# Kernel optimization log

Hardware: AMD Instinct MI355X
Metric: run time of the kernel (lower is better)

## Reference

```python
import jax, jax.numpy as jnp
import numpy as np

IN_DIM, HIDDEN, OUT_DIM = 784, 2048, 10
BATCH = 16384
KEEP = 0.1  # 1 - sparsity


def setup_inputs() -> dict:
    key = jax.random.key(0)
    ks = jax.random.split(key, 16)
    s1 = 1.0 / np.sqrt(IN_DIM)
    sh = 1.0 / np.sqrt(HIDDEN)
    inp = {
        "x": jax.random.normal(ks[0], (BATCH, IN_DIM), dtype=jnp.float32),
        # weights stored as (out, in) like nn.Linear
        "W1": jax.random.uniform(ks[1], (HIDDEN, IN_DIM), jnp.float32, -s1, s1),
        "b1": jax.random.uniform(ks[2], (HIDDEN,), jnp.float32, -s1, s1),
        "W2": jax.random.uniform(ks[3], (HIDDEN, HIDDEN), jnp.float32, -sh, sh),
        "b2": jax.random.uniform(ks[4], (HIDDEN,), jnp.float32, -sh, sh),
        "W3": jax.random.uniform(ks[5], (HIDDEN, HIDDEN), jnp.float32, -sh, sh),
        "b3": jax.random.uniform(ks[6], (HIDDEN,), jnp.float32, -sh, sh),
        "W4": jax.random.uniform(ks[7], (HIDDEN, HIDDEN), jnp.float32, -sh, sh),
        "b4": jax.random.uniform(ks[8], (HIDDEN,), jnp.float32, -sh, sh),
        "W5": jax.random.uniform(ks[9], (OUT_DIM, HIDDEN), jnp.float32, -sh, sh),
        "b5": jax.random.uniform(ks[10], (OUT_DIM,), jnp.float32, -sh, sh),
        "m1": jax.random.bernoulli(ks[11], KEEP, (HIDDEN, IN_DIM)),
        "m2": jax.random.bernoulli(ks[12], KEEP, (HIDDEN, HIDDEN)),
        "m3": jax.random.bernoulli(ks[13], KEEP, (HIDDEN, HIDDEN)),
        "m4": jax.random.bernoulli(ks[14], KEEP, (HIDDEN, HIDDEN)),
    }
    return inp


def _sparse_linear(x, W, b, m):
    # masked linear: y = x @ (W*m)^T + b
    Wm = W * m.astype(W.dtype)
    return x @ Wm.T + b


def reference(x, W1, b1, W2, b2, W3, b3, W4, b4, W5, b5, m1, m2, m3, m4):
    h = x.reshape(x.shape[0], -1)
    h = jax.nn.relu(_sparse_linear(h, W1, b1, m1))
    h = jax.nn.relu(_sparse_linear(h, W2, b2, m2))
    h = jax.nn.relu(_sparse_linear(h, W3, b3, m3))
    h = jax.nn.relu(_sparse_linear(h, W4, b4, m4))
    return h @ W5.T + b5
```

## Files before the change

kernel.cpp:

```cpp
#include <hip/hip_runtime.h>
#include <hip/hip_bf16.h>
#include <hip/hip_fp16.h>

#define BATCH 16384
#define HID   2048
#define IND   784
#define INDP  896
#define OUTD  10

typedef _Float16 f16;
typedef __attribute__((ext_vector_type(8))) _Float16 f16x8;
typedef __attribute__((ext_vector_type(4))) float f32x4;

__global__ void mask_detect(const unsigned char* __restrict__ p, int nbytes,
                            int* __restrict__ flags) {
    int acc = 0;
    for (int i = blockIdx.x * blockDim.x + threadIdx.x; i < nbytes;
         i += gridDim.x * blockDim.x) {
        unsigned char b = p[i];
        if (b > 1) acc |= 2;
        else if (b != 0 && (i & 3) != 0) acc |= 1;
    }
    if (acc) atomicOr(flags, acc);
}

__global__ void prep_cast(const float* __restrict__ W,
                          const void* __restrict__ Mk,
                          const int* __restrict__ flags,
                          f16* __restrict__ out,
                          int rin, int kin, int kout, int total) {
    int idx = blockIdx.x * blockDim.x + threadIdx.x;
    if (idx >= total) return;
    int r = idx / kout, c = idx - r * kout;
    float v = 0.f;
    if (r < rin && c < kin) {
        v = W[(size_t)r * kin + c];
        if (Mk) {
            size_t mi = (size_t)r * kin + c;
            bool byteMode = (*flags == 1);
            bool keep = byteMode ? (((const unsigned char*)Mk)[mi] != 0)
                                 : (((const unsigned int*)Mk)[mi] != 0u);
            if (!keep) v = 0.f;
        }
    }
    out[idx] = (f16)v;
}

__device__ __forceinline__ void gload_lds16(const f16* g, f16* l) {
    __builtin_amdgcn_global_load_lds(
        (const __attribute__((address_space(1))) unsigned int*)g,
        (__attribute__((address_space(3))) unsigned int*)l,
        16, 0, 0);
}

#define BAR()    __builtin_amdgcn_s_barrier()
#define SCHED()  __builtin_amdgcn_sched_barrier(0)
#define WAITV4() asm volatile("s_waitcnt vmcnt(4)" ::: "memory")
#define WAITV8() asm volatile("s_waitcnt vmcnt(8)" ::: "memory")
#define WAITL0() asm volatile("s_waitcnt lgkmcnt(0)" ::: "memory")

template<bool RELU>
__global__ __launch_bounds__(512, 2) void gemm8p(
    const f16* __restrict__ A, const f16* __restrict__ B,
    const float* __restrict__ bias, f16* __restrict__ C,
    int N, int K) {
    __shared__ f16 As[2 * 2 * 256 * 32];
    __shared__ f16 Bs[2 * 2 * 256 * 32];

    int nbn = N >> 8;
    int nwg = gridDim.x;
    int cpx = nwg >> 3;
    int bid = blockIdx.x;
    int swz = (bid & 7) * cpx + (bid >> 3);
    int bm = swz / nbn, bn = swz % nbn;

    int tid = threadIdx.x;
    int w = tid >> 6, lane = tid & 63;
    int wr = w >> 2, wc = w & 3;
    int l15 = lane & 15, l4 = lane >> 4;

    const f16* Ag = A + (size_t)bm * 256 * K;
    const f16* Bg = B + (size_t)bn * 256 * K;

    int r0 = tid >> 2, s0 = tid & 3;
    int c0 = (s0 ^ ((r0 >> 1) & 3)) * 8;
    int ldsw0 = (w * 64) * 8;
    int ldsw1 = (512 + w * 64) * 8;

    auto stageA = [&](int buf, int ks, int tk) {
        const f16* s = Ag + (size_t)r0 * K + tk * 64 + ks * 32 + c0;
        gload_lds16(s, As + (buf * 2 + ks) * 8192 + ldsw0);
        const f16* s2 = Ag + (size_t)(128 + r0) * K + tk * 64 + ks * 32 + c0;
        gload_lds16(s2, As + (buf * 2 + ks) * 8192 + ldsw1);
    };
    auto stageB = [&](int buf, int ks, int tk) {
        const f16* s = Bg + (size_t)r0 * K + tk * 64 + ks * 32 + c0;
        gload_lds16(s, Bs + (buf * 2 + ks) * 8192 + ldsw0);
        const f16* s2 = Bg + (size_t)(128 + r0) * K + tk * 64 + ks * 32 + c0;
        gload_lds16(s2, Bs + (buf * 2 + ks) * 8192 + ldsw1);
    };

    int rsw = (l4 ^ ((l15 >> 1) & 3)) * 8;
    auto ldA = [&](f16x8 (&af)[4], int buf, int ks, int mh) {
        int base = (buf * 2 + ks) * 8192;
        #pragma unroll
        for (int m = 0; m < 4; ++m) {
            int row = wr * 128 + (mh * 4 + m) * 16 + l15;
            af[m] = *(const f16x8*)(As + base + row * 32 + rsw);
        }
    };
    auto ldB = [&](f16x8 (&bf)[4], int buf, int ks) {
        int base = (buf * 2 + ks) * 8192;
        #pragma unroll
        for (int n = 0; n < 4; ++n) {
            int row = wc * 64 + n * 16 + l15;
            bf[n] = *(const f16x8*)(Bs + base + row * 32 + rsw);
        }
    };

    f32x4 acc[8][4] = {};
    auto mma = [&](f16x8 (&af)[4], f16x8 (&bf)[4], int mh) {
        __builtin_amdgcn_s_setprio(1);
        #pragma unroll
        for (int m = 0; m < 4; ++m)
            #pragma unroll
            for (int n = 0; n < 4; ++n)
                acc[mh * 4 + m][n] = __builtin_amdgcn_mfma_f32_16x16x32_f16(
                    af[m], bf[n], acc[mh * 4 + m][n], 0, 0, 0);
        __builtin_amdgcn_s_setprio(0);
    };

    int NT = K >> 6, NI = NT >> 1;

    f16x8 A0[4], A1[4], B0[4], B1[4];

    stageA(0, 0, 0); stageB(0, 0, 0); stageA(0, 1, 0); stageB(0, 1, 0);
    stageA(1, 0, 1); stageB(1, 0, 1);
    WAITV8(); SCHED(); BAR();
    ldA(A0, 0, 0, 0); ldB(B0, 0, 0);
    WAITL0(); SCHED();

    for (int it = 0; it < NI; ++it) {
        int t1 = 2 * it + 1, t2 = 2 * it + 2, t3 = 2 * it + 3;
        if (t2 >= NT) t2 = 0;
        if (t3 >= NT) t3 = 0;

        ldA(A1, 0, 0, 1); stageA(1, 1, t1); SCHED();
        mma(A0, B0, 0);
        WAITL0(); WAITV4(); SCHED(); BAR();
        ldA(A0, 0, 1, 0); ldB(B1, 0, 1); stageB(1, 1, t1); SCHED();
        mma(A1, B0, 1);
        WAITL0(); SCHED(); BAR();
        ldA(A1, 0, 1, 1); stageA(0, 0, t2); SCHED();
        mma(A0, B1, 0);
        WAITL0(); WAITV4(); SCHED(); BAR();
        ldA(A0, 1, 0, 0); ldB(B0, 1, 0); stageB(0, 0, t2); SCHED();
        mma(A1, B1, 1);
        WAITL0(); SCHED(); BAR();
        ldA(A1, 1, 0, 1); stageA(0, 1, t2); SCHED();
        mma(A0, B0, 0);
        WAITL0(); WAITV4(); SCHED(); BAR();
        ldA(A0, 1, 1, 0); ldB(B1, 1, 1); stageB(0, 1, t2); SCHED();
        mma(A1, B0, 1);
        WAITL0(); SCHED(); BAR();
        ldA(A1, 1, 1, 1); stageA(1, 0, t3); SCHED();
        mma(A0, B1, 0);
        WAITL0(); WAITV4(); SCHED(); BAR();
        ldA(A0, 0, 0, 0); ldB(B0, 0, 0); stageB(1, 0, t3); SCHED();
        mma(A1, B1, 1);
        WAITL0(); SCHED(); BAR();
    }

    #pragma unroll
    for (int nf = 0; nf < 4; ++nf) {
        int j = bn * 256 + wc * 64 + nf * 16 + l15;
        float bv = bias[j];
        #pragma unroll
        for (int mf = 0; mf < 8; ++mf) {
            int i0 = bm * 256 + wr * 128 + mf * 16 + l4 * 4;
            #pragma unroll
            for (int r = 0; r < 4; ++r) {
                float v = acc[mf][nf][r] + bv;
                if (RELU) v = fmaxf(v, 0.f);
                C[(size_t)(i0 + r) * N + j] = (f16)v;
            }
        }
    }
}

__global__ __launch_bounds__(256, 3) void gemm_head(
    const f16* __restrict__ A, const f16* __restrict__ B,
    const float* __restrict__ bias, float* __restrict__ C,
    int K, int Nout) {
    __shared__ f16 As[128 * 64];
    __shared__ f16 Bs[128 * 64];
    int bm = blockIdx.x;
    int t = threadIdx.x;
    int w = t >> 6, lane = t & 63;
    int wm = w >> 1, wn = w & 1;
    int l15 = lane & 15, l4 = lane >> 4;
    const f16* Ag = A + (size_t)bm * 128 * K;
    const f16* Bg = B;
    int rr = w * 8 + (lane >> 3);
    int cc = (lane & 7) * 8;
    f32x4 acc[4][4] = {};
    for (int k0 = 0; k0 < K; k0 += 64) {
        #pragma unroll
        for (int i = 0; i < 4; ++i)
            gload_lds16(Ag + (size_t)(i * 32 + rr) * K + k0 + cc, As + i * 2048 + w * 512);
        #pragma unroll
        for (int i = 0; i < 4; ++i)
            gload_lds16(Bg + (size_t)(i * 32 + rr) * K + k0 + cc, Bs + i * 2048 + w * 512);
        __syncthreads();
        #pragma unroll
        for (int ks = 0; ks < 2; ++ks) {
            f16x8 af[4], bfr[4];
            #pragma unroll
            for (int m = 0; m < 4; ++m)
                af[m] = *(const f16x8*)(As + (wm * 64 + m * 16 + l15) * 64 + ks * 32 + l4 * 8);
            #pragma unroll
            for (int n = 0; n < 4; ++n)
                bfr[n] = *(const f16x8*)(Bs + (wn * 64 + n * 16 + l15) * 64 + ks * 32 + l4 * 8);
            #pragma unroll
            for (int m = 0; m < 4; ++m)
                #pragma unroll
                for (int n = 0; n < 4; ++n)
                    acc[m][n] = __builtin_amdgcn_mfma_f32_16x16x32_f16(af[m], bfr[n], acc[m][n], 0, 0, 0);
        }
        __syncthreads();
    }
    #pragma unroll
    for (int n = 0; n < 4; ++n) {
        int j = wn * 64 + n * 16 + l15;
        bool jok = j < Nout;
        float bv = jok ? bias[j] : 0.f;
        #pragma unroll
        for (int m = 0; m < 4; ++m) {
            int i0 = bm * 128 + wm * 64 + m * 16 + l4 * 4;
            #pragma unroll
            for (int r = 0; r < 4; ++r) {
                if (jok) C[(size_t)(i0 + r) * Nout + j] = acc[m][n][r] + bv;
            }
        }
    }
}

extern "C" void kernel_launch(void* const* d_in, const int* in_sizes, int n_in,
                              void* d_out, int out_size, void* d_ws, size_t ws_size,
                              hipStream_t stream) {
    const float* x  = (const float*)d_in[0];
    const float* W1 = (const float*)d_in[1];
    const float* b1 = (const float*)d_in[2];
    const float* W2 = (const float*)d_in[3];
    const float* b2 = (const float*)d_in[4];
    const float* W3 = (const float*)d_in[5];
    const float* b3 = (const float*)d_in[6];
    const float* W4 = (const float*)d_in[7];
    const float* b4 = (const float*)d_in[8];
    const float* W5 = (const float*)d_in[9];
    const float* b5 = (const float*)d_in[10];
    const void* m1 = d_in[11];
    const void* m2 = d_in[12];
    const void* m3 = d_in[13];
    const void* m4 = d_in[14];

    char* ws = (char*)d_ws;
    size_t off = 0;
    auto alloc = [&](size_t b) { char* p = ws + off; off += (b + 255) & ~(size_t)255; return p; };
    f16* xb  = (f16*)alloc((size_t)BATCH * INDP * 2);
    f16* w1b = (f16*)alloc((size_t)HID * INDP * 2);
    f16* w2b = (f16*)alloc((size_t)HID * HID * 2);
    f16* w3b = (f16*)alloc((size_t)HID * HID * 2);
    f16* w4b = (f16*)alloc((size_t)HID * HID * 2);
    f16* w5b = (f16*)alloc((size_t)128 * HID * 2);
    f16* h1  = (f16*)alloc((size_t)BATCH * HID * 2);
    f16* h2  = (f16*)alloc((size_t)BATCH * HID * 2);
    int* flags = (int*)alloc(256);

    hipMemsetAsync(flags, 0, sizeof(int), stream);
    mask_detect<<<64, 256, 0, stream>>>((const unsigned char*)m1, 262144, flags);

    auto prep = [&](const float* src, const void* mk, f16* dst,
                    int rin, int kin, int kout, int rout) {
        int total = rout * kout;
        prep_cast<<<(total + 255) / 256, 256, 0, stream>>>(src, mk, flags, dst,
                                                           rin, kin, kout, total);
    };
    prep(x,  nullptr, xb,  BATCH, IND, INDP, BATCH);
    prep(W1, m1,      w1b, HID,   IND, INDP, HID);
    prep(W2, m2,      w2b, HID,   HID, HID,  HID);
    prep(W3, m3,      w3b, HID,   HID, HID,  HID);
    prep(W4, m4,      w4b, HID,   HID, HID,  HID);
    prep(W5, nullptr, w5b, OUTD,  HID, HID,  128);

    int g8 = (BATCH / 256) * (HID / 256);
    gemm8p<true><<<g8, 512, 0, stream>>>(xb, w1b, b1, h1, HID, INDP);
    gemm8p<true><<<g8, 512, 0, stream>>>(h1, w2b, b2, h2, HID, HID);
    gemm8p<true><<<g8, 512, 0, stream>>>(h2, w3b, b3, h1, HID, HID);
    gemm8p<true><<<g8, 512, 0, stream>>>(h1, w4b, b4, h2, HID, HID);
    gemm_head<<<BATCH / 128, 256, 0, stream>>>(h2, w5b, b5, (float*)d_out, HID, OUTD);
}
```

Baseline: 562.4 us.

## Use 4-wave 256x256 GEMM workgroups with 128x128 per-wave tiles

Rewrites the main GEMM kernel from 8 waves (each computing a 128x64 sub-tile) to 4 waves each computing a 128x128 sub-tile of the same 256x256 block tile. Each thread now issues four global-to-LDS loads per stage instead of two, and the vmcnt waits are adjusted to match. The goal is more MFMA work per LDS fragment read and fewer waves contending for barriers. In exchange, accumulator register use doubles (256 fp32 per lane), occupancy drops to one workgroup of four waves per CU, and there is less latency hiding.

```diff
diff --git a/kernel.cpp b/kernel.cpp
--- a/kernel.cpp
+++ b/kernel.cpp
@@ -55,12 +55,11 @@
 
 #define BAR()    __builtin_amdgcn_s_barrier()
 #define SCHED()  __builtin_amdgcn_sched_barrier(0)
-#define WAITV4() asm volatile("s_waitcnt vmcnt(4)" ::: "memory")
 #define WAITV8() asm volatile("s_waitcnt vmcnt(8)" ::: "memory")
 #define WAITL0() asm volatile("s_waitcnt lgkmcnt(0)" ::: "memory")
 
 template<bool RELU>
-__global__ __launch_bounds__(512, 2) void gemm8p(
+__global__ __launch_bounds__(256, 1) void gemm4w(
     const f16* __restrict__ A, const f16* __restrict__ B,
     const float* __restrict__ bias, f16* __restrict__ C,
     int N, int K) {
@@ -76,7 +75,7 @@
 
     int tid = threadIdx.x;
     int w = tid >> 6, lane = tid & 63;
-    int wr = w >> 2, wc = w & 3;
+    int wr = w >> 1, wc = w & 1;
     int l15 = lane & 15, l4 = lane >> 4;
 
     const f16* Ag = A + (size_t)bm * 256 * K;
@@ -84,20 +83,18 @@
 
     int r0 = tid >> 2, s0 = tid & 3;
     int c0 = (s0 ^ ((r0 >> 1) & 3)) * 8;
-    int ldsw0 = (w * 64) * 8;
-    int ldsw1 = (512 + w * 64) * 8;
 
     auto stageA = [&](int buf, int ks, int tk) {
-        const f16* s = Ag + (size_t)r0 * K + tk * 64 + ks * 32 + c0;
-        gload_lds16(s, As + (buf * 2 + ks) * 8192 + ldsw0);
-        const f16* s2 = Ag + (size_t)(128 + r0) * K + tk * 64 + ks * 32 + c0;
-        gload_lds16(s2, As + (buf * 2 + ks) * 8192 + ldsw1);
+        #pragma unroll
+        for (int j = 0; j < 4; ++j)
+            gload_lds16(Ag + (size_t)(j * 64 + r0) * K + tk * 64 + ks * 32 + c0,
+                        As + (buf * 2 + ks) * 8192 + j * 2048 + w * 512);
     };
     auto stageB = [&](int buf, int ks, int tk) {
-        const f16* s = Bg + (size_t)r0 * K + tk * 64 + ks * 32 + c0;
-        gload_lds16(s, Bs + (buf * 2 + ks) * 8192 + ldsw0);
-        const f16* s2 = Bg + (size_t)(128 + r0) * K + tk * 64 + ks * 32 + c0;
-        gload_lds16(s2, Bs + (buf * 2 + ks) * 8192 + ldsw1);
+        #pragma unroll
+        for (int j = 0; j < 4; ++j)
+            gload_lds16(Bg + (size_t)(j * 64 + r0) * K + tk * 64 + ks * 32 + c0,
+                        Bs + (buf * 2 + ks) * 8192 + j * 2048 + w * 512);
     };
 
     int rsw = (l4 ^ ((l15 >> 1) & 3)) * 8;
@@ -109,22 +106,22 @@
             af[m] = *(const f16x8*)(As + base + row * 32 + rsw);
         }
     };
-    auto ldB = [&](f16x8 (&bf)[4], int buf, int ks) {
+    auto ldB = [&](f16x8 (&bf)[8], int buf, int ks) {
         int base = (buf * 2 + ks) * 8192;
         #pragma unroll
-        for (int n = 0; n < 4; ++n) {
-            int row = wc * 64 + n * 16 + l15;
+        for (int n = 0; n < 8; ++n) {
+            int row = wc * 128 + n * 16 + l15;
             bf[n] = *(const f16x8*)(Bs + base + row * 32 + rsw);
         }
     };
 
-    f32x4 acc[8][4] = {};
-    auto mma = [&](f16x8 (&af)[4], f16x8 (&bf)[4], int mh) {
+    f32x4 acc[8][8] = {};
+    auto mma = [&](f16x8 (&af)[4], f16x8 (&bf)[8], int mh) {
         __builtin_amdgcn_s_setprio(1);
         #pragma unroll
         for (int m = 0; m < 4; ++m)
             #pragma unroll
-            for (int n = 0; n < 4; ++n)
+            for (int n = 0; n < 8; ++n)
                 acc[mh * 4 + m][n] = __builtin_amdgcn_mfma_f32_16x16x32_f16(
                     af[m], bf[n], acc[mh * 4 + m][n], 0, 0, 0);
         __builtin_amdgcn_s_setprio(0);
@@ -132,7 +129,7 @@
 
     int NT = K >> 6, NI = NT >> 1;
 
-    f16x8 A0[4], A1[4], B0[4], B1[4];
+    f16x8 A0[4], A1[4], B0[8], B1[8];
 
     stageA(0, 0, 0); stageB(0, 0, 0); stageA(0, 1, 0); stageB(0, 1, 0);
     stageA(1, 0, 1); stageB(1, 0, 1);
@@ -147,33 +144,33 @@
 
         ldA(A1, 0, 0, 1); stageA(1, 1, t1); SCHED();
         mma(A0, B0, 0);
-        WAITL0(); WAITV4(); SCHED(); BAR();
+        WAITL0(); WAITV8(); SCHED(); BAR();
         ldA(A0, 0, 1, 0); ldB(B1, 0, 1); stageB(1, 1, t1); SCHED();
         mma(A1, B0, 1);
         WAITL0(); SCHED(); BAR();
         ldA(A1, 0, 1, 1); stageA(0, 0, t2); SCHED();
         mma(A0, B1, 0);
-        WAITL0(); WAITV4(); SCHED(); BAR();
+        WAITL0(); WAITV8(); SCHED(); BAR();
         ldA(A0, 1, 0, 0); ldB(B0, 1, 0); stageB(0, 0, t2); SCHED();
         mma(A1, B1, 1);
         WAITL0(); SCHED(); BAR();
         ldA(A1, 1, 0, 1); stageA(0, 1, t2); SCHED();
         mma(A0, B0, 0);
-        WAITL0(); WAITV4(); SCHED(); BAR();
+        WAITL0(); WAITV8(); SCHED(); BAR();
         ldA(A0, 1, 1, 0); ldB(B1, 1, 1); stageB(0, 1, t2); SCHED();
         mma(A1, B0, 1);
         WAITL0(); SCHED(); BAR();
         ldA(A1, 1, 1, 1); stageA(1, 0, t3); SCHED();
         mma(A0, B1, 0);
-        WAITL0(); WAITV4(); SCHED(); BAR();
+        WAITL0(); WAITV8(); SCHED(); BAR();
         ldA(A0, 0, 0, 0); ldB(B0, 0, 0); stageB(1, 0, t3); SCHED();
         mma(A1, B1, 1);
         WAITL0(); SCHED(); BAR();
     }
 
     #pragma unroll
-    for (int nf = 0; nf < 4; ++nf) {
-        int j = bn * 256 + wc * 64 + nf * 16 + l15;
+    for (int nf = 0; nf < 8; ++nf) {
+        int j = bn * 256 + wc * 128 + nf * 16 + l15;
         float bv = bias[j];
         #pragma unroll
         for (int mf = 0; mf < 8; ++mf) {
@@ -293,10 +290,10 @@
     prep(W4, m4,      w4b, HID,   HID, HID,  HID);
     prep(W5, nullptr, w5b, OUTD,  HID, HID,  128);
 
-    int g8 = (BATCH / 256) * (HID / 256);
-    gemm8p<true><<<g8, 512, 0, stream>>>(xb, w1b, b1, h1, HID, INDP);
-    gemm8p<true><<<g8, 512, 0, stream>>>(h1, w2b, b2, h2, HID, HID);
-    gemm8p<true><<<g8, 512, 0, stream>>>(h2, w3b, b3, h1, HID, HID);
-    gemm8p<true><<<g8, 512, 0, stream>>>(h1, w4b, b4, h2, HID, HID);
+    int g4 = (BATCH / 256) * (HID / 256);
+    gemm4w<true><<<g4, 256, 0, stream>>>(xb, w1b, b1, h1, HID, INDP);
+    gemm4w<true><<<g4, 256, 0, stream>>>(h1, w2b, b2, h2, HID, HID);
+    gemm4w<true><<<g4, 256, 0, stream>>>(h2, w3b, b3, h1, HID, HID);
+    gemm4w<true><<<g4, 256, 0, stream>>>(h1, w4b, b4, h2, HID, HID);
     gemm_head<<<BATCH / 128, 256, 0, stream>>>(h2, w5b, b5, (float*)d_out, HID, OUTD);
 }
```

Measured after the change: 604.2 us. 1.07x slower.

## Reorder GEMM main loop to issue MFMAs before next LDS fragment reads

Applied to the files above, without the earlier changes.

Restructures the software-pipelined main loop of the fp16 MFMA GEMM so each phase runs its MFMAs first and then issues the LDS fragment reads and global-to-LDS stages for the next phase. It also preloads both A halves in the prologue and drops the explicit lgkmcnt(0) waits, leaving LDS-read waits to the compiler. The aim is more overlap of LDS reads and global loads with MFMA work and fewer full stalls per phase. Without the explicit LDS-read waits before barriers, a wave's pending fragment reads could race with other waves' async writes into the same buffer.

```diff
diff --git a/kernel.cpp b/kernel.cpp
--- a/kernel.cpp
+++ b/kernel.cpp
@@ -57,7 +57,6 @@
 #define SCHED()  __builtin_amdgcn_sched_barrier(0)
 #define WAITV4() asm volatile("s_waitcnt vmcnt(4)" ::: "memory")
 #define WAITV8() asm volatile("s_waitcnt vmcnt(8)" ::: "memory")
-#define WAITL0() asm volatile("s_waitcnt lgkmcnt(0)" ::: "memory")
 
 template<bool RELU>
 __global__ __launch_bounds__(512, 2) void gemm8p(
@@ -88,16 +87,16 @@
     int ldsw1 = (512 + w * 64) * 8;
 
     auto stageA = [&](int buf, int ks, int tk) {
-        const f16* s = Ag + (size_t)r0 * K + tk * 64 + ks * 32 + c0;
-        gload_lds16(s, As + (buf * 2 + ks) * 8192 + ldsw0);
-        const f16* s2 = Ag + (size_t)(128 + r0) * K + tk * 64 + ks * 32 + c0;
-        gload_lds16(s2, As + (buf * 2 + ks) * 8192 + ldsw1);
+        gload_lds16(Ag + (size_t)r0 * K + tk * 64 + ks * 32 + c0,
+                    As + (buf * 2 + ks) * 8192 + ldsw0);
+        gload_lds16(Ag + (size_t)(128 + r0) * K + tk * 64 + ks * 32 + c0,
+                    As + (buf * 2 + ks) * 8192 + ldsw1);
     };
     auto stageB = [&](int buf, int ks, int tk) {
-        const f16* s = Bg + (size_t)r0 * K + tk * 64 + ks * 32 + c0;
-        gload_lds16(s, Bs + (buf * 2 + ks) * 8192 + ldsw0);
-        const f16* s2 = Bg + (size_t)(128 + r0) * K + tk * 64 + ks * 32 + c0;
-        gload_lds16(s2, Bs + (buf * 2 + ks) * 8192 + ldsw1);
+        gload_lds16(Bg + (size_t)r0 * K + tk * 64 + ks * 32 + c0,
+                    Bs + (buf * 2 + ks) * 8192 + ldsw0);
+        gload_lds16(Bg + (size_t)(128 + r0) * K + tk * 64 + ks * 32 + c0,
+                    Bs + (buf * 2 + ks) * 8192 + ldsw1);
     };
 
     int rsw = (l4 ^ ((l15 >> 1) & 3)) * 8;
@@ -132,43 +131,43 @@
 
     int NT = K >> 6, NI = NT >> 1;
 
-    f16x8 A0[4], A1[4], B0[4], B1[4];
+    f16x8 Aa[4], Ab[4], Ba[4], Bb[4];
 
     stageA(0, 0, 0); stageB(0, 0, 0); stageA(0, 1, 0); stageB(0, 1, 0);
     stageA(1, 0, 1); stageB(1, 0, 1);
     WAITV8(); SCHED(); BAR();
-    ldA(A0, 0, 0, 0); ldB(B0, 0, 0);
-    WAITL0(); SCHED();
+    ldA(Aa, 0, 0, 0); ldB(Bb, 0, 0); ldA(Ab, 0, 0, 1);
+    WAITV4(); SCHED(); BAR();
 
     for (int it = 0; it < NI; ++it) {
         int t1 = 2 * it + 1, t2 = 2 * it + 2, t3 = 2 * it + 3;
         if (t2 >= NT) t2 = 0;
         if (t3 >= NT) t3 = 0;
 
-        ldA(A1, 0, 0, 1); stageA(1, 1, t1); SCHED();
-        mma(A0, B0, 0);
-        WAITL0(); WAITV4(); SCHED(); BAR();
-        ldA(A0, 0, 1, 0); ldB(B1, 0, 1); stageB(1, 1, t1); SCHED();
-        mma(A1, B0, 1);
-        WAITL0(); SCHED(); BAR();
-        ldA(A1, 0, 1, 1); stageA(0, 0, t2); SCHED();
-        mma(A0, B1, 0);
-        WAITL0(); WAITV4(); SCHED(); BAR();
-        ldA(A0, 1, 0, 0); ldB(B0, 1, 0); stageB(0, 0, t2); SCHED();
-        mma(A1, B1, 1);
-        WAITL0(); SCHED(); BAR();
-        ldA(A1, 1, 0, 1); stageA(0, 1, t2); SCHED();
-        mma(A0, B0, 0);
-        WAITL0(); WAITV4(); SCHED(); BAR();
-        ldA(A0, 1, 1, 0); ldB(B1, 1, 1); stageB(0, 1, t2); SCHED();
-        mma(A1, B0, 1);
-        WAITL0(); SCHED(); BAR();
-        ldA(A1, 1, 1, 1); stageA(1, 0, t3); SCHED();
-        mma(A0, B1, 0);
-        WAITL0(); WAITV4(); SCHED(); BAR();
-        ldA(A0, 0, 0, 0); ldB(B0, 0, 0); stageB(1, 0, t3); SCHED();
-        mma(A1, B1, 1);
-        WAITL0(); SCHED(); BAR();
+        mma(Aa, Bb, 0); SCHED();
+        ldA(Aa, 0, 1, 0); ldB(Ba, 0, 1); stageA(1, 1, t1);
+        SCHED(); BAR();
+        mma(Ab, Bb, 1); SCHED();
+        ldA(Ab, 0, 1, 1); stageB(1, 1, t1);
+        WAITV4(); SCHED(); BAR();
+        mma(Aa, Ba, 0); SCHED();
+        ldA(Aa, 1, 0, 0); ldB(Bb, 1, 0); stageA(0, 0, t2);
+        SCHED(); BAR();
+        mma(Ab, Ba, 1); SCHED();
+        ldA(Ab, 1, 0, 1); stageB(0, 0, t2);
+        WAITV4(); SCHED(); BAR();
+        mma(Aa, Bb, 0); SCHED();
+        ldA(Aa, 1, 1, 0); ldB(Ba, 1, 1); stageA(0, 1, t2);
+        SCHED(); BAR();
+        mma(Ab, Bb, 1); SCHED();
+        ldA(Ab, 1, 1, 1); stageB(0, 1, t2);
+        WAITV4(); SCHED(); BAR();
+        mma(Aa, Ba, 0); SCHED();
+        ldA(Aa, 0, 0, 0); ldB(Bb, 0, 0); stageA(1, 0, t3);
+        SCHED(); BAR();
+        mma(Ab, Ba, 1); SCHED();
+        ldA(Ab, 0, 0, 1); stageB(1, 0, t3);
+        WAITV4(); SCHED(); BAR();
     }
 
     #pragma unroll
```

Measured after the change: 538.9 us. 4.2% less time.
